# Kernel tuning notes

Measured on AMD Instinct MI355X. Metric: run time of the kernel, lower is better.

Reference implementation:

```python
import jax, jax.numpy as jnp
import numpy as np

D = 1024      # hidden_size
FF = 4096     # ff_inner_dim = 4 * D
E = 8         # num_experts
K = 2         # moe_top_k
B, L = 4, 1024


def setup_inputs() -> dict:
    key = jax.random.key(0)
    ks = jax.random.split(key, 12)
    s = 0.02  # weight init scale
    return {
        "x": jax.random.normal(ks[0], (B, L, D), jnp.float32),
        "W_gate": jax.random.normal(ks[1], (D, E), jnp.float32) * s,
        "W1": jax.random.normal(ks[2], (E, D, FF), jnp.float32) * s,
        "b1": jnp.zeros((E, FF), jnp.float32),
        "W2": jax.random.normal(ks[3], (E, FF, D), jnp.float32) * s,
        "b2": jnp.zeros((E, D), jnp.float32),
        "Ws1": jax.random.normal(ks[4], (D, FF), jnp.float32) * s,
        "bs1": jnp.zeros((FF,), jnp.float32),
        "Ws2": jax.random.normal(ks[5], (FF, D), jnp.float32) * s,
        "bs2": jnp.zeros((D,), jnp.float32),
    }


def _gelu(h):
    # torch F.gelu default = exact (erf) gelu
    return jax.nn.gelu(h, approximate=False)


def reference(x, W_gate, W1, b1, W2, b2, Ws1, bs1, Ws2, bs2):
    Bx, Lx, Dx = x.shape
    xf = x.reshape(-1, Dx)                       # [T, D]
    logits = xf @ W_gate                         # [T, E]
    probs = jax.nn.softmax(logits, axis=-1)
    top_v, top_i = jax.lax.top_k(probs, K)       # [T, K]
    top_v = top_v / jnp.sum(top_v, axis=-1, keepdims=True)
    # dense combine weights: [T, E], zero for unselected experts
    combine = jnp.sum(jax.nn.one_hot(top_i, E, dtype=xf.dtype) * top_v[..., None], axis=1)

    out = jnp.zeros_like(xf)
    for e in range(E):  # fixed small expert loop, unrolled under jit
        h = _gelu(xf @ W1[e] + b1[e])            # [T, FF]
        out = out + combine[:, e:e + 1] * (h @ W2[e] + b2[e])

    shared = _gelu(xf @ Ws1 + bs1) @ Ws2 + bs2   # [T, D]
    return (out + shared).reshape(Bx, Lx, Dx)
```

## Files before the change

kernel.cpp:

```cpp
#include <hip/hip_runtime.h>
#include <hip/hip_bf16.h>

typedef unsigned short ushort_t;
typedef __attribute__((ext_vector_type(4))) float f32x4;
typedef __attribute__((ext_vector_type(8))) short bf16x8;
typedef __attribute__((ext_vector_type(8))) unsigned short us8;

#define T_TOK 4096
#define D_DIM 1024
#define FF_DIM 4096
#define NE 8
#define ESTRIDE 4194304L

__device__ __forceinline__ unsigned short f2bf(float f) {
  __hip_bfloat16 h = __float2bfloat16(f);
  return __builtin_bit_cast(unsigned short, h);
}
__device__ __forceinline__ float gelu_f(float v) {
  return 0.5f * v * (1.0f + erff(v * 0.70710678118654752440f));
}

__global__ void gate_kernel(const float* __restrict__ x, const float* __restrict__ Wg,
                            int* __restrict__ cnt, int* __restrict__ tok,
                            float* __restrict__ wof, int* __restrict__ rankof) {
  const int t = blockIdx.x;
  const int lane = threadIdx.x;
  const float* xr = x + (long)t * D_DIM;
  float acc[NE];
#pragma unroll
  for (int e = 0; e < NE; e++) acc[e] = 0.f;
#pragma unroll
  for (int i = 0; i < 16; i++) {
    int d = i * 64 + lane;
    float xv = xr[d];
    const float* wr = Wg + d * NE;
#pragma unroll
    for (int e = 0; e < NE; e++) acc[e] += xv * wr[e];
  }
#pragma unroll
  for (int off = 32; off > 0; off >>= 1) {
#pragma unroll
    for (int e = 0; e < NE; e++) acc[e] += __shfl_xor(acc[e], off, 64);
  }
  if (lane == 0) {
    int i0 = 0;
#pragma unroll
    for (int e = 1; e < NE; e++) if (acc[e] > acc[i0]) i0 = e;
    int i1 = -1;
#pragma unroll
    for (int e = 0; e < NE; e++) {
      if (e == i0) continue;
      if (i1 < 0 || acc[e] > acc[i1]) i1 = e;
    }
    float e1 = expf(acc[i1] - acc[i0]);
    float w0 = 1.f / (1.f + e1);
    float w1 = e1 * w0;
    int s0 = atomicAdd(&cnt[i0], 1);
    tok[i0 * T_TOK + s0] = t; wof[i0 * T_TOK + s0] = w0; rankof[i0 * T_TOK + s0] = 0;
    int s1 = atomicAdd(&cnt[i1], 1);
    tok[i1 * T_TOK + s1] = t; wof[i1 * T_TOK + s1] = w1; rankof[i1 * T_TOK + s1] = 1;
    tok[8 * T_TOK + t] = t; wof[8 * T_TOK + t] = 1.f; rankof[8 * T_TOK + t] = 0;
  }
}

__global__ void scan_kernel(int* cnt, int* base) {
  if (threadIdx.x == 0 && blockIdx.x == 0) {
    int s = 0;
    for (int e = 0; e < NE; e++) { base[e] = s; s += cnt[e]; }
    base[8] = s;
    cnt[8] = T_TOK;
  }
}

__global__ void build_queue_kernel(const int* __restrict__ cnt,
                                   unsigned int* __restrict__ q1,
                                   unsigned int* __restrict__ q2,
                                   int* __restrict__ nq) {
  const int e = blockIdx.x;
  int off1 = 0, off2 = 0, tot1 = 0, tot2 = 0, M = 0;
  for (int i = 0; i < 9; i++) {
    int c = (i == 8) ? T_TOK : cnt[i];
    int m = (c + 127) >> 7;
    if (i < e) { off1 += m * 32; off2 += m * 8; }
    if (i == e) M = m;
    tot1 += m * 32; tot2 += m * 8;
  }
  for (int i = threadIdx.x; i < M * 32; i += 256) {
    int my = i >> 5, nx = i & 31;
    int ms = my >> 2, mi = my & 3, ns = nx >> 3, ni = nx & 7;
    int h = M - ms * 4; if (h > 4) h = 4;
    int pos = ms * 128 + ns * (h * 8) + mi * 8 + ni;
    q1[off1 + pos] = ((unsigned)e << 16) | ((unsigned)my << 8) | (unsigned)nx;
  }
  for (int i = threadIdx.x; i < M * 8; i += 256) {
    int my = i >> 3, nx = i & 7;
    int ms = my >> 1, mi = my & 1, ns = nx >> 1, ni = nx & 1;
    int h = M - ms * 2; if (h > 2) h = 2;
    int pos = ms * 16 + ns * (h * 2) + mi * 2 + ni;
    q2[off2 + pos] = ((unsigned)e << 16) | ((unsigned)my << 8) | (unsigned)nx;
  }
  if (e == 0 && threadIdx.x == 0) { nq[0] = tot1; nq[1] = tot2; }
}

__global__ void cvt_x_kernel(const float* __restrict__ src, ushort_t* __restrict__ dst) {
  long i = ((long)blockIdx.x * 256 + threadIdx.x) * 8;
  float4 v0 = *(const float4*)(src + i);
  float4 v1 = *(const float4*)(src + i + 4);
  us8 o;
  o[0] = f2bf(v0.x); o[1] = f2bf(v0.y); o[2] = f2bf(v0.z); o[3] = f2bf(v0.w);
  o[4] = f2bf(v1.x); o[5] = f2bf(v1.y); o[6] = f2bf(v1.z); o[7] = f2bf(v1.w);
  *(us8*)(dst + i) = o;
}

__global__ void tcvt_kernel(const float* __restrict__ W, const float* __restrict__ Wsh,
                            ushort_t* __restrict__ dst, int R, int C) {
  const float* src = (blockIdx.z == 8) ? Wsh : (W + (long)blockIdx.z * R * C);
  ushort_t* d = dst + (long)blockIdx.z * R * C;
  const int r0 = blockIdx.y * 128, c0 = blockIdx.x * 64;
  __shared__ ushort_t tile[64][136];
  const int t = threadIdx.x;
#pragma unroll
  for (int i = 0; i < 8; i++) {
    int lin = t + i * 256;
    int r = lin >> 4;
    int c = (lin & 15) * 4;
    float4 v = *(const float4*)(src + (long)(r0 + r) * C + c0 + c);
    tile[c + 0][r] = f2bf(v.x);
    tile[c + 1][r] = f2bf(v.y);
    tile[c + 2][r] = f2bf(v.z);
    tile[c + 3][r] = f2bf(v.w);
  }
  __syncthreads();
#pragma unroll
  for (int i = 0; i < 4; i++) {
    int lin = t + i * 256;
    int cc = lin >> 4, rp = lin & 15;
    us8 v = *(const us8*)&tile[cc][rp * 8];
    *(us8*)(d + (long)(c0 + cc) * R + r0 + rp * 8) = v;
  }
}

template <int K, int N, int PHASE>
__global__ __launch_bounds__(256, 2) void gemm_kernel(
    const ushort_t* __restrict__ Abase, const ushort_t* __restrict__ WT,
    const float* __restrict__ bias_e, const float* __restrict__ bias_s,
    const int* __restrict__ cnt, const int* __restrict__ base,
    const int* __restrict__ tok, const float* __restrict__ wof,
    const int* __restrict__ rankof,
    const unsigned int* __restrict__ q, const int* __restrict__ nq_all,
    ushort_t* __restrict__ He, float* __restrict__ ybuf, float* __restrict__ out) {
  const int nq = nq_all[PHASE - 1];
  const int tid = threadIdx.x;
  const int w = tid >> 6, lane = tid & 63;
  const int wm = w >> 1, wn = w & 1;
  const int lr = lane & 15, lg = lane >> 4;

  __shared__ ushort_t lds_u[2 * 16384];
  char* const lds = (char*)lds_u;

  const int srow8 = tid >> 3;
  const int g8 = (tid & 7) ^ (srow8 & 7);

  int offA[4], offB[4];
#pragma unroll
  for (int m = 0; m < 4; m++) {
    int r = wm * 64 + m * 16 + lr;
    offA[m] = r * 128 + ((lg ^ (r & 7)) << 4);
  }
#pragma unroll
  for (int n = 0; n < 4; n++) {
    int r = wn * 64 + n * 16 + lr;
    offB[n] = r * 128 + ((lg ^ (r & 7)) << 4);
  }

  constexpr int NT = K / 64;
  const int chunk = gridDim.x >> 3;
  const int vbid = (blockIdx.x & 7) * chunk + (blockIdx.x >> 3);

#define STAGE(buf_, kk_)                                                         \
  do {                                                                           \
    char* dd_ = lds + (buf_) * 32768 + tid * 16;                                 \
    _Pragma("unroll")                                                            \
    for (int i_ = 0; i_ < 4; i_++) {                                             \
      __builtin_amdgcn_global_load_lds(                                          \
          (const __attribute__((address_space(1))) void*)(pA[i_] + (kk_)),       \
          (__attribute__((address_space(3))) void*)(dd_ + i_ * 4096), 16, 0, 0); \
      __builtin_amdgcn_global_load_lds(                                          \
          (const __attribute__((address_space(1))) void*)(pB[i_] + (kk_)),       \
          (__attribute__((address_space(3))) void*)(dd_ + 16384 + i_ * 4096),    \
          16, 0, 0);                                                             \
    }                                                                            \
  } while (0)

  for (int it = vbid; it < nq; it += gridDim.x) {
    const unsigned int item = q[it];
    const int e = item >> 16;
    const int m0 = ((item >> 8) & 0xff) * 128;
    const int n0 = (item & 0xff) * 128;
    const int count = cnt[e];

    const ushort_t* pA[4];
    const ushort_t* pB[4];
#pragma unroll
    for (int i = 0; i < 4; i++) {
      int rr = m0 + i * 32 + srow8;
      int rc = (rr < count) ? rr : 0;
      long arow;
      if (PHASE == 1) arow = tok[e * T_TOK + rc];
      else            arow = (long)base[e] + rc;
      pA[i] = Abase + arow * (long)K + g8 * 8;
      pB[i] = WT + (long)e * ESTRIDE + (long)(n0 + i * 32 + srow8) * K + g8 * 8;
    }

    f32x4 acc[4][4] = {};

    __builtin_amdgcn_s_barrier();
    asm volatile("" ::: "memory");
    STAGE(0, 0);

    for (int t = 0; t < NT; t++) {
      if (t + 1 < NT) {
        STAGE((t + 1) & 1, (t + 1) * 64);
        asm volatile("s_waitcnt vmcnt(8)" ::: "memory");
      } else {
        asm volatile("s_waitcnt vmcnt(0)" ::: "memory");
      }
      __builtin_amdgcn_s_barrier();
      asm volatile("" ::: "memory");

      const char* aB = lds + (t & 1) * 32768;
      const char* bB = aB + 16384;
#pragma unroll
      for (int kk = 0; kk < 2; kk++) {
        const int kx = kk << 6;
        bf16x8 av[4], bv[4];
#pragma unroll
        for (int m = 0; m < 4; m++)
          av[m] = *(const bf16x8*)(aB + (offA[m] ^ kx));
#pragma unroll
        for (int n = 0; n < 4; n++)
          bv[n] = *(const bf16x8*)(bB + (offB[n] ^ kx));
#pragma unroll
        for (int m = 0; m < 4; m++)
#pragma unroll
          for (int n = 0; n < 4; n++)
            acc[m][n] = __builtin_amdgcn_mfma_f32_16x16x32_bf16(av[m], bv[n], acc[m][n], 0, 0, 0);
      }
      __builtin_amdgcn_s_barrier();
      asm volatile("" ::: "memory");
    }

    const float* bias = (e == NE) ? bias_s : (bias_e + (long)e * N);
#pragma unroll
    for (int m = 0; m < 4; m++) {
#pragma unroll
      for (int j = 0; j < 4; j++) {
        int rloc = wm * 64 + m * 16 + lg * 4 + j;
        int rr = m0 + rloc;
        if (rr >= count) continue;
        if (PHASE == 1) {
          long orow = (long)base[e] + rr;
#pragma unroll
          for (int n = 0; n < 4; n++) {
            int col = n0 + wn * 64 + n * 16 + lr;
            float v = acc[m][n][j] + bias[col];
            He[orow * FF_DIM + col] = f2bf(gelu_f(v));
          }
        } else {
          int tt = tok[e * T_TOK + rr];
          if (e == NE) {
#pragma unroll
            for (int n = 0; n < 4; n++) {
              int col = n0 + wn * 64 + n * 16 + lr;
              out[(long)tt * D_DIM + col] = acc[m][n][j] + bias[col];
            }
          } else {
            float wgt = wof[e * T_TOK + rr];
            int rk = rankof[e * T_TOK + rr];
            float* dst = ybuf + (long)rk * ((long)T_TOK * D_DIM) + (long)tt * D_DIM;
#pragma unroll
            for (int n = 0; n < 4; n++) {
              int col = n0 + wn * 64 + n * 16 + lr;
              dst[col] = wgt * (acc[m][n][j] + bias[col]);
            }
          }
        }
      }
    }
  }
#undef STAGE
}

__global__ void final_add_kernel(float* __restrict__ out, const float* __restrict__ ybuf) {
  long i = ((long)blockIdx.x * 256 + threadIdx.x) * 4;
  float4 a = *(const float4*)(out + i);
  float4 b = *(const float4*)(ybuf + i);
  float4 c = *(const float4*)(ybuf + (long)T_TOK * D_DIM + i);
  a.x += b.x + c.x; a.y += b.y + c.y; a.z += b.z + c.z; a.w += b.w + c.w;
  *(float4*)(out + i) = a;
}

extern "C" void kernel_launch(void* const* d_in, const int* in_sizes, int n_in,
                              void* d_out, int out_size, void* d_ws, size_t ws_size,
                              hipStream_t stream) {
  (void)in_sizes; (void)n_in; (void)out_size; (void)ws_size;
  const float* x   = (const float*)d_in[0];
  const float* Wg  = (const float*)d_in[1];
  const float* W1  = (const float*)d_in[2];
  const float* b1  = (const float*)d_in[3];
  const float* W2  = (const float*)d_in[4];
  const float* b2  = (const float*)d_in[5];
  const float* Ws1 = (const float*)d_in[6];
  const float* bs1 = (const float*)d_in[7];
  const float* Ws2 = (const float*)d_in[8];
  const float* bs2 = (const float*)d_in[9];
  float* out = (float*)d_out;

  char* ws = (char*)d_ws;
  int*      cnt    = (int*)(ws + 0);
  int*      base   = (int*)(ws + 64);
  int*      tok    = (int*)(ws + 256);
  float*    wof    = (float*)(ws + 256 + 147456);
  int*      rankof = (int*)(ws + 256 + 2 * 147456);
  ushort_t* Xbf    = (ushort_t*)(ws + 442624);
  ushort_t* W1T    = (ushort_t*)(ws + 8831232);
  ushort_t* W2T    = (ushort_t*)(ws + 84328704);
  ushort_t* He     = (ushort_t*)(ws + 159826176);
  int*      nq     = (int*)(ws + 260489472);
  unsigned int* q1 = (unsigned int*)(ws + 260489536);
  unsigned int* q2 = (unsigned int*)(ws + 260489536 + 32768);
  float*    ybuf   = (float*)(ws + 261538048);

  hipMemsetAsync(cnt, 0, 64, stream);
  gate_kernel<<<T_TOK, 64, 0, stream>>>(x, Wg, cnt, tok, wof, rankof);
  scan_kernel<<<1, 64, 0, stream>>>(cnt, base);
  build_queue_kernel<<<9, 256, 0, stream>>>(cnt, q1, q2, nq);
  cvt_x_kernel<<<2048, 256, 0, stream>>>(x, Xbf);
  tcvt_kernel<<<dim3(64, 8, 9), 256, 0, stream>>>(W1, Ws1, W1T, 1024, 4096);
  tcvt_kernel<<<dim3(16, 32, 9), 256, 0, stream>>>(W2, Ws2, W2T, 4096, 1024);
  gemm_kernel<1024, 4096, 1><<<3328, 256, 0, stream>>>(
      Xbf, W1T, b1, bs1, cnt, base, tok, wof, rankof, q1, nq, He, ybuf, out);
  gemm_kernel<4096, 1024, 2><<<832, 256, 0, stream>>>(
      He, W2T, b2, bs2, cnt, base, tok, wof, rankof, q2, nq, He, ybuf, out);
  final_add_kernel<<<4096, 256, 0, stream>>>(out, ybuf);
}
```

Before: 547.9 us.

## Enlarge GEMM tiles to 256x256 with 1024-thread blocks and K-step 32

The grouped expert GEMMs move from 128x128 tiles with 256 threads to 256x256 tiles with 16 waves per block. The K step per stage drops from 64 to 32, and the LDS swizzle becomes a rotation over 4 column groups. Work queues are rebuilt for the larger tiles, and launches become persistent grids of 512 and 256 blocks. The aim is more operand reuse per global load and fewer tiles to schedule. In exchange it brings more tail waste on partially filled expert M-tiles, occupancy of one block per CU, and only one MFMA k-substep per barrier pair, which adds sync overhead.

```diff
diff --git a/kernel.cpp b/kernel.cpp
--- a/kernel.cpp
+++ b/kernel.cpp
@@ -80,23 +80,21 @@
   int off1 = 0, off2 = 0, tot1 = 0, tot2 = 0, M = 0;
   for (int i = 0; i < 9; i++) {
     int c = (i == 8) ? T_TOK : cnt[i];
-    int m = (c + 127) >> 7;
-    if (i < e) { off1 += m * 32; off2 += m * 8; }
+    int m = (c + 255) >> 8;
+    if (i < e) { off1 += m * 16; off2 += m * 4; }
     if (i == e) M = m;
-    tot1 += m * 32; tot2 += m * 8;
-  }
-  for (int i = threadIdx.x; i < M * 32; i += 256) {
-    int my = i >> 5, nx = i & 31;
-    int ms = my >> 2, mi = my & 3, ns = nx >> 3, ni = nx & 7;
-    int h = M - ms * 4; if (h > 4) h = 4;
-    int pos = ms * 128 + ns * (h * 8) + mi * 8 + ni;
+    tot1 += m * 16; tot2 += m * 4;
+  }
+  for (int i = threadIdx.x; i < M * 16; i += 256) {
+    int my = i >> 4, nx = i & 15;
+    int ms = my >> 1, mi = my & 1, ns = nx >> 2, ni = nx & 3;
+    int h = M - ms * 2; if (h > 2) h = 2;
+    int pos = ms * 32 + ns * (h * 4) + mi * 4 + ni;
     q1[off1 + pos] = ((unsigned)e << 16) | ((unsigned)my << 8) | (unsigned)nx;
   }
-  for (int i = threadIdx.x; i < M * 8; i += 256) {
-    int my = i >> 3, nx = i & 7;
-    int ms = my >> 1, mi = my & 1, ns = nx >> 1, ni = nx & 1;
-    int h = M - ms * 2; if (h > 2) h = 2;
-    int pos = ms * 16 + ns * (h * 2) + mi * 2 + ni;
+  for (int i = threadIdx.x; i < M * 4; i += 256) {
+    int my = i >> 2, nx = i & 3;
+    int pos = nx * M + my;
     q2[off2 + pos] = ((unsigned)e << 16) | ((unsigned)my << 8) | (unsigned)nx;
   }
   if (e == 0 && threadIdx.x == 0) { nq[0] = tot1; nq[1] = tot2; }
@@ -141,7 +139,7 @@
 }
 
 template <int K, int N, int PHASE>
-__global__ __launch_bounds__(256, 2) void gemm_kernel(
+__global__ __launch_bounds__(1024, 1) void gemm_kernel(
     const ushort_t* __restrict__ Abase, const ushort_t* __restrict__ WT,
     const float* __restrict__ bias_e, const float* __restrict__ bias_s,
     const int* __restrict__ cnt, const int* __restrict__ base,
@@ -152,65 +150,56 @@
   const int nq = nq_all[PHASE - 1];
   const int tid = threadIdx.x;
   const int w = tid >> 6, lane = tid & 63;
-  const int wm = w >> 1, wn = w & 1;
+  const int wm = w >> 2, wn = w & 3;
   const int lr = lane & 15, lg = lane >> 4;
 
   __shared__ ushort_t lds_u[2 * 16384];
   char* const lds = (char*)lds_u;
 
-  const int srow8 = tid >> 3;
-  const int g8 = (tid & 7) ^ (srow8 & 7);
+  const int srow = tid >> 2;
+  const int cg = ((tid & 3) - (srow >> 1)) & 3;
 
   int offA[4], offB[4];
 #pragma unroll
   for (int m = 0; m < 4; m++) {
     int r = wm * 64 + m * 16 + lr;
-    offA[m] = r * 128 + ((lg ^ (r & 7)) << 4);
+    offA[m] = r * 64 + (((lg + (r >> 1)) & 3) << 4);
   }
 #pragma unroll
   for (int n = 0; n < 4; n++) {
     int r = wn * 64 + n * 16 + lr;
-    offB[n] = r * 128 + ((lg ^ (r & 7)) << 4);
-  }
-
-  constexpr int NT = K / 64;
+    offB[n] = r * 64 + (((lg + (r >> 1)) & 3) << 4);
+  }
+
+  constexpr int NT = K / 32;
   const int chunk = gridDim.x >> 3;
   const int vbid = (blockIdx.x & 7) * chunk + (blockIdx.x >> 3);
 
-#define STAGE(buf_, kk_)                                                         \
-  do {                                                                           \
-    char* dd_ = lds + (buf_) * 32768 + tid * 16;                                 \
-    _Pragma("unroll")                                                            \
-    for (int i_ = 0; i_ < 4; i_++) {                                             \
-      __builtin_amdgcn_global_load_lds(                                          \
-          (const __attribute__((address_space(1))) void*)(pA[i_] + (kk_)),       \
-          (__attribute__((address_space(3))) void*)(dd_ + i_ * 4096), 16, 0, 0); \
-      __builtin_amdgcn_global_load_lds(                                          \
-          (const __attribute__((address_space(1))) void*)(pB[i_] + (kk_)),       \
-          (__attribute__((address_space(3))) void*)(dd_ + 16384 + i_ * 4096),    \
-          16, 0, 0);                                                             \
-    }                                                                            \
+#define STAGE(buf_, kk_)                                                        \
+  do {                                                                          \
+    char* dd_ = lds + (buf_) * 32768 + tid * 16;                                \
+    __builtin_amdgcn_global_load_lds(                                           \
+        (const __attribute__((address_space(1))) void*)(pA + (kk_)),            \
+        (__attribute__((address_space(3))) void*)(dd_), 16, 0, 0);              \
+    __builtin_amdgcn_global_load_lds(                                           \
+        (const __attribute__((address_space(1))) void*)(pB + (kk_)),            \
+        (__attribute__((address_space(3))) void*)(dd_ + 16384), 16, 0, 0);      \
   } while (0)
 
   for (int it = vbid; it < nq; it += gridDim.x) {
     const unsigned int item = q[it];
     const int e = item >> 16;
-    const int m0 = ((item >> 8) & 0xff) * 128;
-    const int n0 = (item & 0xff) * 128;
+    const int m0 = ((item >> 8) & 0xff) * 256;
+    const int n0 = (item & 0xff) * 256;
     const int count = cnt[e];
 
-    const ushort_t* pA[4];
-    const ushort_t* pB[4];
-#pragma unroll
-    for (int i = 0; i < 4; i++) {
-      int rr = m0 + i * 32 + srow8;
-      int rc = (rr < count) ? rr : 0;
-      long arow;
-      if (PHASE == 1) arow = tok[e * T_TOK + rc];
-      else            arow = (long)base[e] + rc;
-      pA[i] = Abase + arow * (long)K + g8 * 8;
-      pB[i] = WT + (long)e * ESTRIDE + (long)(n0 + i * 32 + srow8) * K + g8 * 8;
-    }
+    int rr = m0 + srow;
+    int rc = (rr < count) ? rr : 0;
+    long arow;
+    if (PHASE == 1) arow = tok[e * T_TOK + rc];
+    else            arow = (long)base[e] + rc;
+    const ushort_t* pA = Abase + arow * (long)K + cg * 8;
+    const ushort_t* pB = WT + (long)e * ESTRIDE + (long)(n0 + srow) * K + cg * 8;
 
     f32x4 acc[4][4] = {};
 
@@ -220,8 +209,8 @@
 
     for (int t = 0; t < NT; t++) {
       if (t + 1 < NT) {
-        STAGE((t + 1) & 1, (t + 1) * 64);
-        asm volatile("s_waitcnt vmcnt(8)" ::: "memory");
+        STAGE((t + 1) & 1, (t + 1) * 32);
+        asm volatile("s_waitcnt vmcnt(2)" ::: "memory");
       } else {
         asm volatile("s_waitcnt vmcnt(0)" ::: "memory");
       }
@@ -230,22 +219,17 @@
 
       const char* aB = lds + (t & 1) * 32768;
       const char* bB = aB + 16384;
-#pragma unroll
-      for (int kk = 0; kk < 2; kk++) {
-        const int kx = kk << 6;
-        bf16x8 av[4], bv[4];
-#pragma unroll
-        for (int m = 0; m < 4; m++)
-          av[m] = *(const bf16x8*)(aB + (offA[m] ^ kx));
+      bf16x8 av[4], bv[4];
+#pragma unroll
+      for (int m = 0; m < 4; m++) av[m] = *(const bf16x8*)(aB + offA[m]);
+#pragma unroll
+      for (int n = 0; n < 4; n++) bv[n] = *(const bf16x8*)(bB + offB[n]);
+#pragma unroll
+      for (int m = 0; m < 4; m++)
 #pragma unroll
         for (int n = 0; n < 4; n++)
-          bv[n] = *(const bf16x8*)(bB + (offB[n] ^ kx));
-#pragma unroll
-        for (int m = 0; m < 4; m++)
-#pragma unroll
-          for (int n = 0; n < 4; n++)
-            acc[m][n] = __builtin_amdgcn_mfma_f32_16x16x32_bf16(av[m], bv[n], acc[m][n], 0, 0, 0);
-      }
+          acc[m][n] = __builtin_amdgcn_mfma_f32_16x16x32_bf16(av[m], bv[n], acc[m][n], 0, 0, 0);
+
       __builtin_amdgcn_s_barrier();
       asm volatile("" ::: "memory");
     }
@@ -256,10 +240,10 @@
 #pragma unroll
       for (int j = 0; j < 4; j++) {
         int rloc = wm * 64 + m * 16 + lg * 4 + j;
-        int rr = m0 + rloc;
-        if (rr >= count) continue;
+        int rrr = m0 + rloc;
+        if (rrr >= count) continue;
         if (PHASE == 1) {
-          long orow = (long)base[e] + rr;
+          long orow = (long)base[e] + rrr;
 #pragma unroll
           for (int n = 0; n < 4; n++) {
             int col = n0 + wn * 64 + n * 16 + lr;
@@ -267,7 +251,7 @@
             He[orow * FF_DIM + col] = f2bf(gelu_f(v));
           }
         } else {
-          int tt = tok[e * T_TOK + rr];
+          int tt = tok[e * T_TOK + rrr];
           if (e == NE) {
 #pragma unroll
             for (int n = 0; n < 4; n++) {
@@ -275,8 +259,8 @@
               out[(long)tt * D_DIM + col] = acc[m][n][j] + bias[col];
             }
           } else {
-            float wgt = wof[e * T_TOK + rr];
-            int rk = rankof[e * T_TOK + rr];
+            float wgt = wof[e * T_TOK + rrr];
+            int rk = rankof[e * T_TOK + rrr];
             float* dst = ybuf + (long)rk * ((long)T_TOK * D_DIM) + (long)tt * D_DIM;
 #pragma unroll
             for (int n = 0; n < 4; n++) {
@@ -338,9 +322,9 @@
   cvt_x_kernel<<<2048, 256, 0, stream>>>(x, Xbf);
   tcvt_kernel<<<dim3(64, 8, 9), 256, 0, stream>>>(W1, Ws1, W1T, 1024, 4096);
   tcvt_kernel<<<dim3(16, 32, 9), 256, 0, stream>>>(W2, Ws2, W2T, 4096, 1024);
-  gemm_kernel<1024, 4096, 1><<<3328, 256, 0, stream>>>(
+  gemm_kernel<1024, 4096, 1><<<512, 1024, 0, stream>>>(
       Xbf, W1T, b1, bs1, cnt, base, tok, wof, rankof, q1, nq, He, ybuf, out);
-  gemm_kernel<4096, 1024, 2><<<832, 256, 0, stream>>>(
+  gemm_kernel<4096, 1024, 2><<<256, 1024, 0, stream>>>(
       He, W2T, b2, bs2, cnt, base, tok, wof, rankof, q2, nq, He, ybuf, out);
   final_add_kernel<<<4096, 256, 0, stream>>>(out, ybuf);
 }
```

New measurement: 524.3 us. 1.04x faster.
